# Performance work log

Hardware: AMD Instinct MI355X
Metric: run time of the kernel (lower is better)

## Reference

```python
import jax, jax.numpy as jnp
import numpy as np

# norse LIF/LI defaults, v_th overridden to 0.4 in the module
DT = 0.001
TAU_SYN_INV = 200.0
TAU_MEM_INV = 100.0
V_TH = 0.4
SEQ_LEN = 128
ALPHA = 100.0  # superspike surrogate slope (fwd = heaviside)


def heaviside(x):
    return (x > 0).astype(x.dtype)


def _linear_init(k, out_d, in_d):
    bound = 1.0 / np.sqrt(in_d)
    kw, kb = jax.random.split(k)
    W = jax.random.uniform(kw, (out_d, in_d), jnp.float32, -bound, bound)
    b = jax.random.uniform(kb, (out_d,), jnp.float32, -bound, bound)
    return W, b


def setup_inputs() -> dict:
    key = jax.random.key(0)
    ks = jax.random.split(key, 5)
    B = 4096
    x = jax.random.normal(ks[0], (B, 3, 32, 32), jnp.float32)
    W1, b1 = _linear_init(ks[1], 1536, 3072)
    W2, b2 = _linear_init(ks[2], 256, 1536)
    W3, b3 = _linear_init(ks[3], 10, 256)
    # per-timestep additive noise (0.001 * randn in the original)
    noise = jax.random.normal(ks[4], (SEQ_LEN, B, 10), jnp.float32)
    return dict(x=x, W1=W1, b1=b1, W2=W2, b2=b2, W3=W3, b3=b3, noise=noise)


def reference(x, W1, b1, W2, b2, W3, b3, noise):
    B = x.shape[0]
    xf = x.reshape(B, -1)                      # Flatten
    inp1 = xf @ W1.T + b1                      # constant across timesteps -> hoist

    def lif_step(v, i, inp):
        # norse lif_step: decay v with old i, decay i, spike, reset, then add input current
        v_dec = v + DT * TAU_MEM_INV * (-v + i)
        i_dec = i * (1.0 - DT * TAU_SYN_INV)
        z = heaviside(v_dec - V_TH)
        return z, (1.0 - z) * v_dec, i_dec + inp

    def step(carry, n_t):
        v1, i1, v2, i2, vl, il = carry
        z1, v1, i1 = lif_step(v1, i1, inp1)
        a2 = z1 @ W2.T + b2
        z2, v2, i2 = lif_step(v2, i2, a2)
        a3 = z2 @ W3.T + b3
        # norse li_step: v integrates old i; i decays then receives input
        vl = vl + DT * TAU_MEM_INV * (-vl + il)
        il = il * (1.0 - DT * TAU_SYN_INV) + a3
        return (v1, i1, v2, i2, vl, il), vl + 0.001 * n_t

    init = (
        jnp.zeros((B, 1536), x.dtype), jnp.zeros((B, 1536), x.dtype),
        jnp.zeros((B, 256), x.dtype), jnp.zeros((B, 256), x.dtype),
        jnp.zeros((B, 10), x.dtype), jnp.zeros((B, 10), x.dtype),
    )
    _, voltages = jax.lax.scan(step, init, noise)  # [SEQ_LEN, B, 10]
    return jnp.max(voltages, axis=0)
```

## Files before the change

### kernel.cpp

```cpp
#include <hip/hip_runtime.h>

#define BSZ   4096
#define NIN   3072
#define N1    1536
#define N2    256
#define NO    10
#define SEQ   128
#define CH    16
#define NCHUNK (SEQ/CH)

#define DVM  0.1f
#define DIS  0.8f
#define VTH  0.4f

#define W2S1 2.0090963e-04f
#define W2S2 7.9098279e-07f

#define S1X 4.7244094e-02f
#define S2X 1.8600037e-04f
#define S3X 7.3228492e-07f
#define S1W 1.4206453e-04f
#define S2W 5.5931704e-07f
#define S3W 2.2020356e-09f

#define OFF_INP1 0
#define OFF_A2   0
#define OFF_A3   0
#define OFF_XF   67108864
#define OFF_Z1   67108864
#define OFF_W1F  167772160
#define OFF_V2   167772160
#define OFF_I2   171966464
#define OFF_Z2   176160768
#define OFF_W2F  196083712

typedef short bf16x8 __attribute__((ext_vector_type(8)));
typedef float f32x4  __attribute__((ext_vector_type(4)));
typedef int   i32x4  __attribute__((ext_vector_type(4)));

__device__ __forceinline__ void gload_lds16(const unsigned short* g, unsigned short* l) {
    __builtin_amdgcn_global_load_lds(
        (const __attribute__((address_space(1))) unsigned int*)g,
        (__attribute__((address_space(3))) unsigned int*)l, 16, 0, 0);
}

__device__ __forceinline__ int q8(float v, float inv) {
    int a = (int)rintf(v * inv);
    return a > 127 ? 127 : (a < -127 ? -127 : a);
}

__global__ __launch_bounds__(256) void prep_x_i8(
        const float* __restrict__ x, signed char* __restrict__ xq) {
    const int idx = blockIdx.x * 256 + threadIdx.x;
    const int lane = idx & 63;
    const int m16 = (idx >> 6) & 255;
    const int ks  = idx >> 14;
    const int row = m16 * 16 + (lane & 15);
    const int k0  = ks * 64 + (lane >> 4) * 16;
    const float* src = x + (size_t)row * NIN + k0;
    union { signed char c[16]; i32x4 v; } q1, q2, q3;
    #pragma unroll
    for (int j = 0; j < 16; j++) {
        float v = src[j];
        v = fminf(fmaxf(v, -6.f), 6.f);
        int a = q8(v, 1.0f / S1X);
        float r1 = fmaf((float)(-a), S1X, v);
        int b = q8(r1, 1.0f / S2X);
        float r2 = fmaf((float)(-b), S2X, r1);
        int c = q8(r2, 1.0f / S3X);
        q1.c[j] = (signed char)a; q2.c[j] = (signed char)b; q3.c[j] = (signed char)c;
    }
    signed char* dst = xq + (size_t)(ks * 256 + m16) * 3072 + lane * 16;
    *(i32x4*)(dst)        = q1.v;
    *(i32x4*)(dst + 1024) = q2.v;
    *(i32x4*)(dst + 2048) = q3.v;
}

__global__ __launch_bounds__(256) void prep_w1_i8(
        const float* __restrict__ W1, signed char* __restrict__ w1q) {
    const int idx = blockIdx.x * 256 + threadIdx.x;
    const int ks  = idx / 6144;
    const int rem = idx % 6144;
    const int n16 = rem >> 6;
    const int lane = rem & 63;
    const int row = n16 * 16 + (lane & 15);
    const int k0  = ks * 64 + (lane >> 4) * 16;
    const float* src = W1 + (size_t)row * NIN + k0;
    union { signed char c[16]; i32x4 v; } q1, q2, q3;
    #pragma unroll
    for (int j = 0; j < 16; j++) {
        float v = src[j];
        int a = q8(v, 1.0f / S1W);
        float r1 = fmaf((float)(-a), S1W, v);
        int b = q8(r1, 1.0f / S2W);
        float r2 = fmaf((float)(-b), S2W, r1);
        int c = q8(r2, 1.0f / S3W);
        q1.c[j] = (signed char)a; q2.c[j] = (signed char)b; q3.c[j] = (signed char)c;
    }
    signed char* dst = w1q + ((size_t)ks * 12 + (n16 >> 3)) * 24576
                           + (n16 & 7) * 3072 + lane * 16;
    *(i32x4*)(dst)        = q1.v;
    *(i32x4*)(dst + 1024) = q2.v;
    *(i32x4*)(dst + 2048) = q3.v;
}

__global__ __launch_bounds__(256, 3) void gemm1_i8(
        const signed char* __restrict__ xq, const signed char* __restrict__ w1q,
        const float* __restrict__ b1, float* __restrict__ inp1) {
    __shared__ signed char Bs[2][24576];
    const int tx = threadIdx.x;
    const int wave = tx >> 6, lane = tx & 63;
    const int wm = wave >> 1, wn = wave & 1;
    const int ln = lane & 15, ko = lane >> 4;
    const int bid = blockIdx.x;
    const int wg = (bid & 7) * 96 + (bid >> 3);
    const int mtile = wg / 12, ntile = wg % 12;
    const int m16b = mtile * 4 + wm * 2;

    i32x4 acc[2][4][3];
    #pragma unroll
    for (int mt = 0; mt < 2; mt++)
        #pragma unroll
        for (int nt = 0; nt < 4; nt++)
            #pragma unroll
            for (int d = 0; d < 3; d++) acc[mt][nt][d] = (i32x4){0,0,0,0};

    const signed char* xbase = xq + lane * 16;

#define ALOADI(A_, ks_) do {                                                  \
    _Pragma("unroll")                                                         \
    for (int mt_ = 0; mt_ < 2; mt_++)                                         \
        _Pragma("unroll")                                                     \
        for (int d_ = 0; d_ < 3; d_++)                                        \
            A_[mt_][d_] = *(const i32x4*)(xbase +                             \
                (size_t)((ks_) * 256 + m16b + mt_) * 3072 + d_ * 1024);       \
} while (0)

#define STAGEI(ks_, buf_) do {                                                \
    const signed char* s_ = w1q + ((size_t)(ks_) * 12 + ntile) * 24576        \
                                + wave * 6144 + lane * 16;                    \
    signed char* d_ = &Bs[buf_][wave * 6144];                                 \
    _Pragma("unroll")                                                         \
    for (int j_ = 0; j_ < 6; j_++)                                            \
        gload_lds16((const unsigned short*)(s_ + j_ * 1024),                  \
                    (unsigned short*)(d_ + j_ * 1024));                       \
} while (0)

#define COMPI(A_, buf_) do {                                                  \
    _Pragma("unroll")                                                         \
    for (int nt_ = 0; nt_ < 4; nt_++) {                                       \
        const signed char* bp_ = &Bs[buf_][(wn * 4 + nt_) * 3072 + lane * 16];\
        i32x4 e1 = *(const i32x4*)(bp_);                                      \
        i32x4 e2 = *(const i32x4*)(bp_ + 1024);                               \
        i32x4 e3 = *(const i32x4*)(bp_ + 2048);                               \
        _Pragma("unroll")                                                     \
        for (int mt_ = 0; mt_ < 2; mt_++) {                                   \
            acc[mt_][nt_][0] = __builtin_amdgcn_mfma_i32_16x16x64_i8(A_[mt_][0], e1, acc[mt_][nt_][0], 0, 0, 0); \
            acc[mt_][nt_][1] = __builtin_amdgcn_mfma_i32_16x16x64_i8(A_[mt_][0], e2, acc[mt_][nt_][1], 0, 0, 0); \
            acc[mt_][nt_][1] = __builtin_amdgcn_mfma_i32_16x16x64_i8(A_[mt_][1], e1, acc[mt_][nt_][1], 0, 0, 0); \
            acc[mt_][nt_][2] = __builtin_amdgcn_mfma_i32_16x16x64_i8(A_[mt_][0], e3, acc[mt_][nt_][2], 0, 0, 0); \
            acc[mt_][nt_][2] = __builtin_amdgcn_mfma_i32_16x16x64_i8(A_[mt_][1], e2, acc[mt_][nt_][2], 0, 0, 0); \
            acc[mt_][nt_][2] = __builtin_amdgcn_mfma_i32_16x16x64_i8(A_[mt_][2], e1, acc[mt_][nt_][2], 0, 0, 0); \
        }                                                                     \
    }                                                                         \
} while (0)

    i32x4 aA[2][3];
    STAGEI(0, 0);
    __syncthreads();

    for (int ks = 0; ks < 48; ks++) {
        const int buf = ks & 1;
        ALOADI(aA, ks);
        if (ks + 1 < 48) STAGEI(ks + 1, buf ^ 1);
        COMPI(aA, buf);
        __syncthreads();
    }

    const float S11 = S1X * S1W;
    #pragma unroll
    for (int nt = 0; nt < 4; nt++) {
        const int n = ntile * 128 + wn * 64 + nt * 16 + ln;
        const float bias = b1[n];
        #pragma unroll
        for (int mt = 0; mt < 2; mt++) {
            #pragma unroll
            for (int r = 0; r < 4; r++) {
                const int m = mtile * 64 + wm * 32 + mt * 16 + ko * 4 + r;
                float f = (float)acc[mt][nt][0][r]
                        + (1.0f / 254.0f)   * (float)acc[mt][nt][1][r]
                        + (1.0f / 64516.0f) * (float)acc[mt][nt][2][r];
                inp1[(size_t)m * N1 + n] = fmaf(f, S11, bias);
            }
        }
    }
#undef ALOADI
#undef STAGEI
#undef COMPI
}

__global__ __launch_bounds__(256) void lif1_kernel(
        const float* __restrict__ inp1, unsigned long long* __restrict__ z1d) {
    const int b = blockIdx.y;
    const int n = blockIdx.x * 256 + threadIdx.x;
    const int lane = threadIdx.x & 63;
    const int w = n >> 6;
    const float inp = inp1[(size_t)b * N1 + n];
    float v = 0.f, i = 0.f;
    unsigned int u[4];
    #pragma unroll
    for (int s = 0; s < 4; s++) {
        unsigned int acc = 0;
        #pragma unroll
        for (int k = 0; k < 32; k++) {
            float vd = v + DVM * (i - v);
            bool z = (vd - VTH) > 0.f;
            acc = (acc << 1) | (z ? 1u : 0u);
            v = z ? 0.f : vd;
            i = DIS * i + inp;
        }
        u[s] = acc;
    }
    unsigned long long X0 = ((unsigned long long)u[0] << 32) | u[1];
    unsigned long long X1 = ((unsigned long long)u[2] << 32) | u[3];
    #pragma unroll
    for (int s = 0; s < 6; s++) {
        const int j = 32 >> s;
        const unsigned long long m =
            (s == 0) ? 0x00000000FFFFFFFFull :
            (s == 1) ? 0x0000FFFF0000FFFFull :
            (s == 2) ? 0x00FF00FF00FF00FFull :
            (s == 3) ? 0x0F0F0F0F0F0F0F0Full :
            (s == 4) ? 0x3333333333333333ull : 0x5555555555555555ull;
        unsigned long long p0 = __shfl_xor(X0, j, 64);
        unsigned long long p1 = __shfl_xor(X1, j, 64);
        if (lane & j) {
            X0 = (X0 & m) | ((p0 << j) & ~m);
            X1 = (X1 & m) | ((p1 << j) & ~m);
        } else {
            X0 = (X0 & ~m) | ((p0 >> j) & m);
            X1 = (X1 & ~m) | ((p1 >> j) & m);
        }
    }
    unsigned long long Y0 = ((unsigned long long)__builtin_bitreverse32((unsigned int)X0) << 32)
                          | __builtin_bitreverse32((unsigned int)(X0 >> 32));
    unsigned long long Y1 = ((unsigned long long)__builtin_bitreverse32((unsigned int)X1) << 32)
                          | __builtin_bitreverse32((unsigned int)(X1 >> 32));
    const int bg = b >> 7, bl = b & 127;
    unsigned long long* zb = z1d + ((size_t)(bg * 24 + w) * 128) * 128 + bl;
    zb[(size_t)lane * 128]        = Y0;
    zb[(size_t)(64 + lane) * 128] = Y1;
}

__global__ __launch_bounds__(256) void prep_w2_i8(
        const float* __restrict__ W2, signed char* __restrict__ frag) {
    const int idx = blockIdx.x * 256 + threadIdx.x;
    const int lane = idx & 63;
    const int nt8  = (idx >> 6) & 7;
    const int chunk = idx >> 9;
    const int nblk = chunk & 1, w = chunk >> 1;
    const int n = (nblk * 8 + nt8) * 16 + (lane & 15);
    const int k0 = w * 64 + (lane >> 4) * 16;
    const float* src = W2 + (size_t)n * N1 + k0;
    union { signed char c[16]; i32x4 v; } q1, q2;
    #pragma unroll
    for (int j = 0; j < 16; j++) {
        float x = src[j];
        int a = (int)rintf(x * (1.0f / W2S1));
        a = a > 127 ? 127 : (a < -127 ? -127 : a);
        float r = x - (float)a * W2S1;
        int b = (int)rintf(r * (1.0f / W2S2));
        b = b > 127 ? 127 : (b < -127 ? -127 : b);
        q1.c[j] = (signed char)a;
        q2.c[j] = (signed char)b;
    }
    signed char* dst = frag + (size_t)chunk * 16384 + nt8 * 2048 + lane * 16;
    *(i32x4*)(dst)        = q1.v;
    *(i32x4*)(dst + 1024) = q2.v;
}

__global__ __launch_bounds__(256, 2) void gemm2_i8(
        const unsigned long long* __restrict__ z1d,
        const signed char* __restrict__ w2q,
        const float* __restrict__ b2, float* __restrict__ a2, int c) {
    __shared__ signed char Bs[2][16384];
    const int tx = threadIdx.x;
    const int wave = tx >> 6, lane = tx & 63;
    const int wm = wave >> 1, wn = wave & 1;
    const int ko = lane >> 4, ln = lane & 15;
    const int bm = blockIdx.x;
    const int bn = blockIdx.y;
    const int t_l = bm >> 5;
    const int b0 = (bm & 31) * 128 + wm * 64;
    const int t  = c * CH + t_l;

    i32x4 acc[4][4][2];
    #pragma unroll
    for (int mt = 0; mt < 4; mt++)
        #pragma unroll
        for (int nt = 0; nt < 4; nt++)
            #pragma unroll
            for (int d = 0; d < 2; d++) acc[mt][nt][d] = (i32x4){0,0,0,0};

    const int bg = b0 >> 7;
    const size_t zbase2 = ((size_t)(bg * 24) * 128 + t) * 128 + (b0 & 127) + ln;
    const signed char* sgbase = w2q + (size_t)bn * 16384 + wave * 4096 + lane * 16;

    #define STAGE_B(w_, buf_) do {                                           \
        const signed char* s_ = sgbase + (size_t)(w_) * 32768;               \
        signed char* d_ = &Bs[buf_][wave * 4096];                            \
        _Pragma("unroll")                                                    \
        for (int j_ = 0; j_ < 4; j_++)                                       \
            gload_lds16((const unsigned short*)(s_ + j_ * 1024),             \
                        (unsigned short*)(d_ + j_ * 1024));                  \
    } while (0)

    #define LOADZ(Z_, w_) do {                                               \
        _Pragma("unroll")                                                    \
        for (int mt_ = 0; mt_ < 4; mt_++)                                    \
            Z_[mt_] = z1d[zbase2 + (size_t)(w_) * 16384 + mt_ * 16];         \
    } while (0)

    #define COMP(Z_, buf_) do {                                              \
        i32x4 af[4];                                                         \
        _Pragma("unroll")                                                    \
        for (int mt_ = 0; mt_ < 4; mt_++) {                                  \
            unsigned int bits = (unsigned int)(Z_[mt_] >> (ko * 16)) & 0xFFFFu; \
            _Pragma("unroll")                                                \
            for (int j4 = 0; j4 < 4; j4++) {                                 \
                unsigned int nib = (bits >> (j4 * 4)) & 0xFu;                \
                af[mt_][j4] = (int)((nib * 0x00204081u) & 0x01010101u);      \
            }                                                                \
        }                                                                    \
        _Pragma("unroll")                                                    \
        for (int nt_ = 0; nt_ < 4; nt_++) {                                  \
            const signed char* bp_ = &Bs[buf_][(wn * 4 + nt_) * 2048 + lane * 16]; \
            i32x4 bq0 = *(const i32x4*)(bp_);                                \
            i32x4 bq1 = *(const i32x4*)(bp_ + 1024);                         \
            _Pragma("unroll")                                                \
            for (int mt_ = 0; mt_ < 4; mt_++) {                              \
                acc[mt_][nt_][0] = __builtin_amdgcn_mfma_i32_16x16x64_i8(af[mt_], bq0, acc[mt_][nt_][0], 0, 0, 0); \
                acc[mt_][nt_][1] = __builtin_amdgcn_mfma_i32_16x16x64_i8(af[mt_], bq1, acc[mt_][nt_][1], 0, 0, 0); \
            }                                                                \
        }                                                                    \
    } while (0)

    unsigned long long zwA[4], zwB[4];
    LOADZ(zwA, 0);
    STAGE_B(0, 0);
    __syncthreads();

    for (int w = 0; w < 24; w += 2) {
        LOADZ(zwB, w + 1);
        STAGE_B(w + 1, 1);
        COMP(zwA, 0);
        __syncthreads();
        if (w + 2 < 24) {
            LOADZ(zwA, w + 2);
            STAGE_B(w + 2, 0);
        }
        COMP(zwB, 1);
        __syncthreads();
    }

    #pragma unroll
    for (int nt = 0; nt < 4; nt++) {
        const int o = bn * 128 + (wn * 4 + nt) * 16 + ln;
        const float bias = b2[o];
        #pragma unroll
        for (int mt = 0; mt < 4; mt++) {
            #pragma unroll
            for (int r = 0; r < 4; r++) {
                const int brow = b0 + mt * 16 + ko * 4 + r;
                float val = fmaf((float)acc[mt][nt][0][r], W2S1,
                            fmaf((float)acc[mt][nt][1][r], W2S2, bias));
                a2[((size_t)t_l * BSZ + brow) * N2 + o] = val;
            }
        }
    }
    #undef STAGE_B
    #undef LOADZ
    #undef COMP
}

__global__ __launch_bounds__(256) void lif2z_kernel(
        const float* __restrict__ a2, float* __restrict__ v2s, float* __restrict__ i2s,
        unsigned long long* __restrict__ z2bits, int c) {
    const int b = blockIdx.x;
    const int n = threadIdx.x;
    const int wid = n >> 6, lane = n & 63;
    float av[CH];
    #pragma unroll
    for (int tl = 0; tl < CH; tl++)
        av[tl] = a2[((size_t)tl * BSZ + b) * N2 + n];
    float v2, i2;
    if (c == 0) { v2 = 0.f; i2 = 0.f; }
    else { v2 = v2s[(size_t)b * N2 + n]; i2 = i2s[(size_t)b * N2 + n]; }
    #pragma unroll
    for (int tl = 0; tl < CH; tl++) {
        float vd = v2 + DVM * (i2 - v2);
        bool z = (vd - VTH) > 0.f;
        unsigned long long m = __ballot(z);
        if (lane == 0) z2bits[((size_t)(c * CH + tl) * BSZ + b) * 4 + wid] = m;
        v2 = z ? 0.f : vd;
        i2 = DIS * i2 + av[tl];
    }
    v2s[(size_t)b * N2 + n] = v2;
    i2s[(size_t)b * N2 + n] = i2;
}

__global__ __launch_bounds__(256) void gemm3_kernel(
        const unsigned long long* __restrict__ z2bits, const float* __restrict__ W3,
        const float* __restrict__ b3, float* __restrict__ a3) {
    const int idx = blockIdx.x * 256 + threadIdx.x;
    unsigned long long zw[4];
    #pragma unroll
    for (int g = 0; g < 4; g++) zw[g] = z2bits[(size_t)idx * 4 + g];
    float acc[NO];
    #pragma unroll
    for (int o = 0; o < NO; o++) acc[o] = b3[o];
    #pragma unroll
    for (int g = 0; g < 4; g++) {
        unsigned long long wg = zw[g];
        for (int kb = 0; kb < 64; kb++) {
            float bit = (float)((wg >> kb) & 1ull);
            #pragma unroll
            for (int o = 0; o < NO; o++)
                acc[o] = fmaf(bit, W3[o * N2 + g * 64 + kb], acc[o]);
        }
    }
    #pragma unroll
    for (int o = 0; o < NO; o++) a3[(size_t)idx * NO + o] = acc[o];
}

__global__ __launch_bounds__(256) void li_kernel(
        const float* __restrict__ a3, const float* __restrict__ noise,
        float* __restrict__ out) {
    const int idx = blockIdx.x * 256 + threadIdx.x;
    if (idx >= BSZ * NO) return;
    float vl = 0.f, il = 0.f, mx = -1e30f;
    for (int t = 0; t < SEQ; t++) {
        float a = a3[(size_t)t * (BSZ * NO) + idx];
        float vn = vl + DVM * (il - vl);
        il = DIS * il + a;
        vl = vn;
        mx = fmaxf(mx, vl + 0.001f * noise[(size_t)t * (BSZ * NO) + idx]);
    }
    out[idx] = mx;
}

extern "C" void kernel_launch(void* const* d_in, const int* in_sizes, int n_in,
                              void* d_out, int out_size, void* d_ws, size_t ws_size,
                              hipStream_t stream) {
    const float* x     = (const float*)d_in[0];
    const float* W1    = (const float*)d_in[1];
    const float* b1    = (const float*)d_in[2];
    const float* W2    = (const float*)d_in[3];
    const float* b2    = (const float*)d_in[4];
    const float* W3    = (const float*)d_in[5];
    const float* b3    = (const float*)d_in[6];
    const float* noise = (const float*)d_in[7];
    float* out = (float*)d_out;

    char* ws = (char*)d_ws;
    float* inp1 = (float*)(ws + OFF_INP1);
    float* a2   = (float*)(ws + OFF_A2);
    float* a3   = (float*)(ws + OFF_A3);
    signed char* xq  = (signed char*)(ws + OFF_XF);
    signed char* w1q = (signed char*)(ws + OFF_W1F);
    unsigned long long* z1 = (unsigned long long*)(ws + OFF_Z1);
    float* v2 = (float*)(ws + OFF_V2);
    float* i2 = (float*)(ws + OFF_I2);
    unsigned long long* z2 = (unsigned long long*)(ws + OFF_Z2);
    signed char* w2q = (signed char*)(ws + OFF_W2F);

    dim3 blk(256);
    prep_x_i8<<<dim3(3072), blk, 0, stream>>>(x, xq);
    prep_w1_i8<<<dim3(1152), blk, 0, stream>>>(W1, w1q);
    prep_w2_i8<<<dim3(96), blk, 0, stream>>>(W2, w2q);
    gemm1_i8<<<dim3(768), blk, 0, stream>>>(xq, w1q, b1, inp1);
    lif1_kernel<<<dim3(N1/256, BSZ), blk, 0, stream>>>(inp1, z1);
    for (int c = 0; c < NCHUNK; c++) {
        gemm2_i8<<<dim3(512, 2), blk, 0, stream>>>(z1, w2q, b2, a2, c);
        lif2z_kernel<<<dim3(BSZ), blk, 0, stream>>>(a2, v2, i2, z2, c);
    }
    gemm3_kernel<<<dim3(SEQ * BSZ / 256), blk, 0, stream>>>(z2, W3, b3, a3);
    li_kernel<<<dim3((BSZ * NO + 255) / 256), blk, 0, stream>>>(a3, noise, out);
}
```

Baseline: 901.2 us.

## Fuse layer-2 GEMM with LIF recurrence in a persistent time-looping kernel

```diff
diff --git a/kernel.cpp b/kernel.cpp
--- a/kernel.cpp
+++ b/kernel.cpp
@@ -6,8 +6,6 @@
 #define N2    256
 #define NO    10
 #define SEQ   128
-#define CH    16
-#define NCHUNK (SEQ/CH)
 
 #define DVM  0.1f
 #define DIS  0.8f
@@ -24,13 +22,10 @@
 #define S3W 2.2020356e-09f
 
 #define OFF_INP1 0
-#define OFF_A2   0
 #define OFF_A3   0
 #define OFF_XF   67108864
 #define OFF_Z1   67108864
 #define OFF_W1F  167772160
-#define OFF_V2   167772160
-#define OFF_I2   171966464
 #define OFF_Z2   176160768
 #define OFF_W2F  196083712
 
@@ -279,154 +274,128 @@
     *(i32x4*)(dst + 1024) = q2.v;
 }
 
-__global__ __launch_bounds__(256, 2) void gemm2_i8(
+__global__ __launch_bounds__(256, 1) void fused_l2(
         const unsigned long long* __restrict__ z1d,
         const signed char* __restrict__ w2q,
-        const float* __restrict__ b2, float* __restrict__ a2, int c) {
-    __shared__ signed char Bs[2][16384];
+        const float* __restrict__ b2,
+        unsigned int* __restrict__ z2h) {
+    __shared__ signed char Bs[98304];
     const int tx = threadIdx.x;
     const int wave = tx >> 6, lane = tx & 63;
-    const int wm = wave >> 1, wn = wave & 1;
     const int ko = lane >> 4, ln = lane & 15;
-    const int bm = blockIdx.x;
-    const int bn = blockIdx.y;
-    const int t_l = bm >> 5;
-    const int b0 = (bm & 31) * 128 + wm * 64;
-    const int t  = c * CH + t_l;
-
-    i32x4 acc[4][4][2];
-    #pragma unroll
-    for (int mt = 0; mt < 4; mt++)
-        #pragma unroll
-        for (int nt = 0; nt < 4; nt++)
-            #pragma unroll
-            for (int d = 0; d < 2; d++) acc[mt][nt][d] = (i32x4){0,0,0,0};
-
-    const int bg = b0 >> 7;
-    const size_t zbase2 = ((size_t)(bg * 24) * 128 + t) * 128 + (b0 & 127) + ln;
-    const signed char* sgbase = w2q + (size_t)bn * 16384 + wave * 4096 + lane * 16;
-
-    #define STAGE_B(w_, buf_) do {                                           \
-        const signed char* s_ = sgbase + (size_t)(w_) * 32768;               \
-        signed char* d_ = &Bs[buf_][wave * 4096];                            \
-        _Pragma("unroll")                                                    \
-        for (int j_ = 0; j_ < 4; j_++)                                       \
-            gload_lds16((const unsigned short*)(s_ + j_ * 1024),             \
-                        (unsigned short*)(d_ + j_ * 1024));                  \
-    } while (0)
-
-    #define LOADZ(Z_, w_) do {                                               \
-        _Pragma("unroll")                                                    \
-        for (int mt_ = 0; mt_ < 4; mt_++)                                    \
-            Z_[mt_] = z1d[zbase2 + (size_t)(w_) * 16384 + mt_ * 16];         \
-    } while (0)
-
-    #define COMP(Z_, buf_) do {                                              \
-        i32x4 af[4];                                                         \
-        _Pragma("unroll")                                                    \
-        for (int mt_ = 0; mt_ < 4; mt_++) {                                  \
-            unsigned int bits = (unsigned int)(Z_[mt_] >> (ko * 16)) & 0xFFFFu; \
-            _Pragma("unroll")                                                \
-            for (int j4 = 0; j4 < 4; j4++) {                                 \
-                unsigned int nib = (bits >> (j4 * 4)) & 0xFu;                \
-                af[mt_][j4] = (int)((nib * 0x00204081u) & 0x01010101u);      \
-            }                                                                \
-        }                                                                    \
-        _Pragma("unroll")                                                    \
-        for (int nt_ = 0; nt_ < 4; nt_++) {                                  \
-            const signed char* bp_ = &Bs[buf_][(wn * 4 + nt_) * 2048 + lane * 16]; \
-            i32x4 bq0 = *(const i32x4*)(bp_);                                \
-            i32x4 bq1 = *(const i32x4*)(bp_ + 1024);                         \
-            _Pragma("unroll")                                                \
-            for (int mt_ = 0; mt_ < 4; mt_++) {                              \
-                acc[mt_][nt_][0] = __builtin_amdgcn_mfma_i32_16x16x64_i8(af[mt_], bq0, acc[mt_][nt_][0], 0, 0, 0); \
-                acc[mt_][nt_][1] = __builtin_amdgcn_mfma_i32_16x16x64_i8(af[mt_], bq1, acc[mt_][nt_][1], 0, 0, 0); \
-            }                                                                \
-        }                                                                    \
-    } while (0)
-
-    unsigned long long zwA[4], zwB[4];
-    LOADZ(zwA, 0);
-    STAGE_B(0, 0);
+    const int btile = blockIdx.x & 63;
+    const int otile = blockIdx.x >> 6;
+    const int o0 = otile * 32;
+
+    {
+        const int nblk = otile >> 2, nt8_0 = (otile & 3) * 2;
+        const signed char* s0 = w2q + (size_t)nblk * 16384 + nt8_0 * 2048 + tx * 16;
+        #pragma unroll 4
+        for (int w = 0; w < 24; w++)
+            gload_lds16((const unsigned short*)(s0 + (size_t)w * 32768),
+                        (unsigned short*)(Bs + w * 4096 + tx * 16));
+    }
     __syncthreads();
 
-    for (int w = 0; w < 24; w += 2) {
-        LOADZ(zwB, w + 1);
-        STAGE_B(w + 1, 1);
-        COMP(zwA, 0);
-        __syncthreads();
-        if (w + 2 < 24) {
-            LOADZ(zwA, w + 2);
-            STAGE_B(w + 2, 0);
-        }
-        COMP(zwB, 1);
-        __syncthreads();
-    }
-
-    #pragma unroll
-    for (int nt = 0; nt < 4; nt++) {
-        const int o = bn * 128 + (wn * 4 + nt) * 16 + ln;
-        const float bias = b2[o];
-        #pragma unroll
-        for (int mt = 0; mt < 4; mt++) {
+    float v2[2][4] = {{0.f,0.f,0.f,0.f},{0.f,0.f,0.f,0.f}};
+    float i2[2][4] = {{0.f,0.f,0.f,0.f},{0.f,0.f,0.f,0.f}};
+    float bb2[2];
+    bb2[0] = b2[o0 + ln];
+    bb2[1] = b2[o0 + 16 + ln];
+
+    const int bg = btile >> 1;
+    const size_t zb0 = (size_t)(bg * 24) * 16384 + (btile & 1) * 64 + wave * 16 + ln;
+    const size_t zoutb = (size_t)btile * 64 + wave * 16;
+
+    i32x4 acc[2][2];
+    #pragma unroll
+    for (int nt = 0; nt < 2; nt++)
+        #pragma unroll
+        for (int d = 0; d < 2; d++) acc[nt][d] = (i32x4){0,0,0,0};
+
+#define LOADZH(Z_, t_, wlo_) do {                                             \
+    _Pragma("unroll")                                                         \
+    for (int w_ = 0; w_ < 12; w_++)                                           \
+        Z_[w_] = z1d[zb0 + (size_t)((wlo_) + w_) * 16384 + (size_t)(t_) * 128]; \
+} while (0)
+
+#define COMPH(Z_, wbase_) do {                                                \
+    _Pragma("unroll")                                                         \
+    for (int w_ = 0; w_ < 12; w_++) {                                         \
+        unsigned int bits_ = (unsigned int)(Z_[w_] >> (ko * 16)) & 0xFFFFu;   \
+        i32x4 af_;                                                            \
+        _Pragma("unroll")                                                     \
+        for (int j4_ = 0; j4_ < 4; j4_++)                                     \
+            af_[j4_] = (int)((((bits_ >> (j4_ * 4)) & 0xFu) * 0x00204081u) & 0x01010101u); \
+        _Pragma("unroll")                                                     \
+        for (int nt_ = 0; nt_ < 2; nt_++) {                                   \
+            const signed char* bp_ = Bs + ((wbase_) + w_) * 4096 + nt_ * 2048 + lane * 16; \
+            i32x4 e1_ = *(const i32x4*)(bp_);                                 \
+            i32x4 e2_ = *(const i32x4*)(bp_ + 1024);                          \
+            acc[nt_][0] = __builtin_amdgcn_mfma_i32_16x16x64_i8(af_, e1_, acc[nt_][0], 0, 0, 0); \
+            acc[nt_][1] = __builtin_amdgcn_mfma_i32_16x16x64_i8(af_, e2_, acc[nt_][1], 0, 0, 0); \
+        }                                                                     \
+    }                                                                         \
+} while (0)
+
+    unsigned long long zwA[12], zwB[12];
+    LOADZH(zwA, 0, 0);
+
+    for (int t = 0; t < SEQ; t++) {
+        LOADZH(zwB, t, 12);
+        COMPH(zwA, 0);
+        if (t + 1 < SEQ) LOADZH(zwA, t + 1, 0);
+        COMPH(zwB, 12);
+
+        bool zz[2][4];
+        #pragma unroll
+        for (int nt = 0; nt < 2; nt++) {
             #pragma unroll
             for (int r = 0; r < 4; r++) {
-                const int brow = b0 + mt * 16 + ko * 4 + r;
-                float val = fmaf((float)acc[mt][nt][0][r], W2S1,
-                            fmaf((float)acc[mt][nt][1][r], W2S2, bias));
-                a2[((size_t)t_l * BSZ + brow) * N2 + o] = val;
+                float a2v = fmaf((float)acc[nt][0][r], W2S1,
+                            fmaf((float)acc[nt][1][r], W2S2, bb2[nt]));
+                float vd = v2[nt][r] + DVM * (i2[nt][r] - v2[nt][r]);
+                bool z = (vd - VTH) > 0.f;
+                zz[nt][r] = z;
+                v2[nt][r] = z ? 0.f : vd;
+                i2[nt][r] = DIS * i2[nt][r] + a2v;
             }
-        }
-    }
-    #undef STAGE_B
-    #undef LOADZ
-    #undef COMP
-}
-
-__global__ __launch_bounds__(256) void lif2z_kernel(
-        const float* __restrict__ a2, float* __restrict__ v2s, float* __restrict__ i2s,
-        unsigned long long* __restrict__ z2bits, int c) {
-    const int b = blockIdx.x;
-    const int n = threadIdx.x;
-    const int wid = n >> 6, lane = n & 63;
-    float av[CH];
-    #pragma unroll
-    for (int tl = 0; tl < CH; tl++)
-        av[tl] = a2[((size_t)tl * BSZ + b) * N2 + n];
-    float v2, i2;
-    if (c == 0) { v2 = 0.f; i2 = 0.f; }
-    else { v2 = v2s[(size_t)b * N2 + n]; i2 = i2s[(size_t)b * N2 + n]; }
-    #pragma unroll
-    for (int tl = 0; tl < CH; tl++) {
-        float vd = v2 + DVM * (i2 - v2);
-        bool z = (vd - VTH) > 0.f;
-        unsigned long long m = __ballot(z);
-        if (lane == 0) z2bits[((size_t)(c * CH + tl) * BSZ + b) * 4 + wid] = m;
-        v2 = z ? 0.f : vd;
-        i2 = DIS * i2 + av[tl];
-    }
-    v2s[(size_t)b * N2 + n] = v2;
-    i2s[(size_t)b * N2 + n] = i2;
+            acc[nt][0] = (i32x4){0,0,0,0};
+            acc[nt][1] = (i32x4){0,0,0,0};
+        }
+        unsigned int* zout = z2h + (size_t)(t * 8 + otile) * BSZ + zoutb;
+        #pragma unroll
+        for (int r = 0; r < 4; r++) {
+            unsigned long long m0 = __ballot(zz[0][r]);
+            unsigned long long m1 = __ballot(zz[1][r]);
+            unsigned int word = (unsigned int)((m0 >> (ko * 16)) & 0xFFFFull)
+                              | ((unsigned int)((m1 >> (ko * 16)) & 0xFFFFull) << 16);
+            if (ln == r) zout[ko * 4 + r] = word;
+        }
+    }
+#undef LOADZH
+#undef COMPH
 }
 
 __global__ __launch_bounds__(256) void gemm3_kernel(
-        const unsigned long long* __restrict__ z2bits, const float* __restrict__ W3,
+        const unsigned int* __restrict__ z2h, const float* __restrict__ W3,
         const float* __restrict__ b3, float* __restrict__ a3) {
     const int idx = blockIdx.x * 256 + threadIdx.x;
-    unsigned long long zw[4];
-    #pragma unroll
-    for (int g = 0; g < 4; g++) zw[g] = z2bits[(size_t)idx * 4 + g];
+    const int t = idx >> 12, b = idx & 4095;
+    unsigned int zw[8];
+    #pragma unroll
+    for (int g = 0; g < 8; g++) zw[g] = z2h[(size_t)(t * 8 + g) * BSZ + b];
     float acc[NO];
     #pragma unroll
     for (int o = 0; o < NO; o++) acc[o] = b3[o];
     #pragma unroll
-    for (int g = 0; g < 4; g++) {
-        unsigned long long wg = zw[g];
-        for (int kb = 0; kb < 64; kb++) {
-            float bit = (float)((wg >> kb) & 1ull);
+    for (int g = 0; g < 8; g++) {
+        unsigned int wg = zw[g];
+        for (int kb = 0; kb < 32; kb++) {
+            float bit = (float)((wg >> kb) & 1u);
             #pragma unroll
             for (int o = 0; o < NO; o++)
-                acc[o] = fmaf(bit, W3[o * N2 + g * 64 + kb], acc[o]);
+                acc[o] = fmaf(bit, W3[o * N2 + g * 32 + kb], acc[o]);
         }
     }
     #pragma unroll
@@ -464,14 +433,11 @@
 
     char* ws = (char*)d_ws;
     float* inp1 = (float*)(ws + OFF_INP1);
-    float* a2   = (float*)(ws + OFF_A2);
     float* a3   = (float*)(ws + OFF_A3);
     signed char* xq  = (signed char*)(ws + OFF_XF);
     signed char* w1q = (signed char*)(ws + OFF_W1F);
     unsigned long long* z1 = (unsigned long long*)(ws + OFF_Z1);
-    float* v2 = (float*)(ws + OFF_V2);
-    float* i2 = (float*)(ws + OFF_I2);
-    unsigned long long* z2 = (unsigned long long*)(ws + OFF_Z2);
+    unsigned int* z2h = (unsigned int*)(ws + OFF_Z2);
     signed char* w2q = (signed char*)(ws + OFF_W2F);
 
     dim3 blk(256);
@@ -480,10 +446,7 @@
     prep_w2_i8<<<dim3(96), blk, 0, stream>>>(W2, w2q);
     gemm1_i8<<<dim3(768), blk, 0, stream>>>(xq, w1q, b1, inp1);
     lif1_kernel<<<dim3(N1/256, BSZ), blk, 0, stream>>>(inp1, z1);
-    for (int c = 0; c < NCHUNK; c++) {
-        gemm2_i8<<<dim3(512, 2), blk, 0, stream>>>(z1, w2q, b2, a2, c);
-        lif2z_kernel<<<dim3(BSZ), blk, 0, stream>>>(a2, v2, i2, z2, c);
-    }
-    gemm3_kernel<<<dim3(SEQ * BSZ / 256), blk, 0, stream>>>(z2, W3, b3, a3);
+    fused_l2<<<dim3(512), blk, 0, stream>>>(z1, w2q, b2, z2h);
+    gemm3_kernel<<<dim3(SEQ * BSZ / 256), blk, 0, stream>>>(z2h, W3, b3, a3);
     li_kernel<<<dim3((BSZ * NO + 255) / 256), blk, 0, stream>>>(a3, noise, out);
 }
```

Measured after the change: 1.022 ms. 1.13x slower.
